# Kernel optimization log

Measured on AMD Instinct MI355X. Metric: run time of the kernel, lower is better.

## Reference

```python
import jax, jax.numpy as jnp
import numpy as np

LOCAL_REGION = 16
GRANULARITY = 2048
INIT_RATIO = 8
EXPAND_RATIO = 2
C = 128
N_LAYERS = 5


def setup_inputs() -> dict:
    key = jax.random.key(0)
    ks = jax.random.split(key, 20)
    g = lambda k, s: jax.random.normal(k, s, dtype=jnp.float32) * 0.05
    z = lambda n: jnp.zeros((n,), jnp.float32)
    return {
        "batch_x": jax.random.normal(ks[0], (1, 16384, 4), dtype=jnp.float32),
        # PT: attr embedding (in_channel=1 -> 128), positional MLP (3->128->128)
        "attr_w": g(ks[1], (1, C)), "attr_b": z(C),
        "pos_w1": g(ks[2], (3, C)), "pos_b1": z(C),
        "pos_w2": g(ks[3], (C, C)), "pos_b2": z(C),
        # 5 self-attention layers over the K-neighborhood
        "wq": g(ks[4], (N_LAYERS, C, C)),
        "wk": g(ks[5], (N_LAYERS, C, C)),
        "wv": g(ks[6], (N_LAYERS, C, C)),
        "wout": g(ks[7], (C, C)), "bout": z(C),
        # mu/sigma head: 128 -> 64 -> 16 -> 2
        "ms_w1": g(ks[8], (C, 64)), "ms_b1": z(64),
        "ms_w2": g(ks[9], (64, 16)), "ms_b2": z(16),
        "ms_w3": g(ks[10], (16, 2)), "ms_b3": z(2),
    }


def _window_schedule(N):
    base = min(N // INIT_RATIO, GRANULARITY)
    win = base
    sched = []
    cursor = base
    while cursor < N:
        win = min(win * EXPAND_RATIO, GRANULARITY)
        sched.append((cursor, min(win, N - cursor)))
        cursor += win
    return sched


def _forward(batch_x, attr_w, attr_b, pos_w1, pos_b1, pos_w2, pos_b2,
             wq, wk, wv, wout, bout, ms_w1, ms_b1, ms_w2, ms_b2, ms_w3, ms_b3):
    B, N, _ = batch_x.shape
    total_bits = jnp.float32(0.0)
    for cur, w in _window_schedule(N):
        context = batch_x[:, :cur, :]
        target = batch_x[:, cur:cur + w, :]
        tg, ta = target[..., :3], target[..., 3:]    # [B,M,3], [B,M,1]
        cg, ca = context[..., :3], context[..., 3:]  # [B,Nc,3], [B,Nc,1]
        # knn_points: brute-force squared distances, K smallest
        d2 = (jnp.sum(tg * tg, -1)[:, :, None] + jnp.sum(cg * cg, -1)[:, None, :]
              - 2.0 * jnp.einsum('bmd,bnd->bmn', tg, cg))  # [B,M,Nc]
        _, idx = jax.lax.top_k(-d2, LOCAL_REGION)            # [B,M,K]
        # knn_gather
        gg = jnp.take_along_axis(cg[:, None], idx[..., None], axis=2)  # [B,M,K,3]
        ga = jnp.take_along_axis(ca[:, None], idx[..., None], axis=2)  # [B,M,K,1]
        # n_scale_ball: center each neighborhood, scale into unit ball
        gg = gg - jnp.mean(gg, axis=2, keepdims=True)
        r = jnp.max(jnp.linalg.norm(gg, axis=-1, keepdims=True), axis=2, keepdims=True)
        gg = gg / jnp.maximum(r, 1e-8)
        # PT: pos-encoded grouped self-attention, max-pool over K
        pos = jax.nn.relu(gg @ pos_w1 + pos_b1) @ pos_w2 + pos_b2  # [B,M,K,C]
        f = ga @ attr_w + attr_b + pos
        for l in range(N_LAYERS):
            q, k, v = f @ wq[l], f @ wk[l], f @ wv[l]
            a = jax.nn.softmax(jnp.einsum('bmkc,bmjc->bmkj', q, k)
                               / jnp.sqrt(jnp.float32(C)), axis=-1)
            f = f + jnp.einsum('bmkj,bmjc->bmkc', a, v)
        feat = jnp.max(f @ wout + bout, axis=2)  # [B,M,C]
        # mu/sigma head
        h = jax.nn.relu(feat @ ms_w1 + ms_b1)
        h = jax.nn.relu(h @ ms_w2 + ms_b2)
        ms = h @ ms_w3 + ms_b3
        mu, sigma = ms[..., :1], jnp.exp(ms[..., 1:])
        # feature_probs_based_mu_sigma: bits under quantized Gaussian
        inv = 1.0 / (sigma * jnp.sqrt(jnp.float32(2.0)))
        probs = 0.5 * (jax.lax.erf((ta + 0.5 - mu) * inv)
                       - jax.lax.erf((ta - 0.5 - mu) * inv))
        total_bits = total_bits + jnp.sum(jnp.clip(-jnp.log2(probs + 1e-10), 0.0, 50.0))
    return total_bits


def reference(batch_x, attr_w, attr_b, pos_w1, pos_b1, pos_w2, pos_b2,
              wq, wk, wv, wout, bout, ms_w1, ms_b1, ms_w2, ms_b2, ms_w3, ms_b3):
    return _forward(batch_x, attr_w, attr_b, pos_w1, pos_b1, pos_w2, pos_b2,
                    wq, wk, wv, wout, bout, ms_w1, ms_b1, ms_w2, ms_b2, ms_w3, ms_b3)
```

## Files before the change

kernel.cpp:

```cpp
#include <hip/hip_runtime.h>
#include <math.h>

#define NPTS 16384
#define WWIN 2048
#define NWIN 7
#define KNB  16
#define CDIM 128
#define NTGT (NPTS - WWIN)
#define TPB  4
#define NBLK (NTGT / TPB)
#define NMAT 12

typedef _Float16 f16;
typedef __attribute__((ext_vector_type(8))) _Float16 f16x8;
typedef __attribute__((ext_vector_type(4))) _Float16 f16x4;
typedef __attribute__((ext_vector_type(2))) _Float16 f16x2;
typedef __attribute__((ext_vector_type(4))) float f32x4;

#define MFMA16(a, b, c) __builtin_amdgcn_mfma_f32_16x16x32_f16((a), (b), (c), 0, 0, 0)

__device__ __forceinline__ unsigned umax_(unsigned a, unsigned b) { return a > b ? a : b; }
__device__ __forceinline__ unsigned umin_(unsigned a, unsigned b) { return a < b ? a : b; }

__global__ void prep_kernel(const float* __restrict__ pos_w2,
                            const float* __restrict__ wq,
                            const float* __restrict__ wk,
                            const float* __restrict__ wv,
                            const float* __restrict__ wout,
                            f16* __restrict__ wt) {
  const int i = blockIdx.x * 256 + threadIdx.x;
  if (i >= NMAT * 16384) return;
  const int mat = i >> 14;
  const int e   = i & 16383;
  const int k   = e >> 7;
  const int n   = e & 127;
  if (mat < 7) {
    const float* src = (mat == 0) ? pos_w2 : (mat <= 5 ? wv + (mat - 1) * 16384 : wout);
    wt[mat * 16384 + n * 128 + k] = (f16)src[k * 128 + n];
  } else {
    const int l = mat - 7;
    const float* qr = wq + l * 16384 + k * 128;
    const float* kr = wk + l * 16384 + n * 128;
    float sacc = 0.f;
#pragma unroll 4
    for (int c = 0; c < 128; ++c) sacc += qr[c] * kr[c];
    wt[mat * 16384 + n * 128 + k] = (f16)sacc;
  }
}

__device__ __forceinline__ f16x8 ldA(const f16* __restrict__ buf, int row0,
                                     int l15, int lg, int kc) {
  const int row = row0 + l15;
  const int col = (kc * 32 + lg * 8) ^ ((row & 7) << 3);
  return *(const f16x8*)(buf + row * 128 + col);
}

__device__ __forceinline__ void stD(f16* __restrict__ buf, int row0, int col0,
                                    int l15, int lg, const f32x4 v) {
#pragma unroll
  for (int r = 0; r < 4; ++r) {
    const int row = row0 + lg * 4 + r;
    const int col = (col0 + l15) ^ ((row & 7) << 3);
    buf[row * 128 + col] = (f16)v[r];
  }
}

__device__ __forceinline__ void zacc(f32x4 (&acc)[4][2]) {
#pragma unroll
  for (int mt = 0; mt < 4; ++mt)
#pragma unroll
    for (int nt = 0; nt < 2; ++nt) acc[mt][nt] = (f32x4){0.f, 0.f, 0.f, 0.f};
}

__device__ __forceinline__ void gemm_tile(const f16* __restrict__ src,
                                          const f16* __restrict__ wmat,
                                          int l15, int lg, int n0,
                                          f32x4 (&acc)[4][2]) {
#pragma unroll
  for (int kc = 0; kc < 4; ++kc) {
    const f16x8 b0 = *(const f16x8*)(wmat + (n0 + l15) * 128 + kc * 32 + lg * 8);
    const f16x8 b1 = *(const f16x8*)(wmat + (n0 + 16 + l15) * 128 + kc * 32 + lg * 8);
#pragma unroll
    for (int mt = 0; mt < 4; ++mt) {
      const f16x8 a = ldA(src, mt * 16, l15, lg, kc);
      acc[mt][0] = MFMA16(a, b0, acc[mt][0]);
      acc[mt][1] = MFMA16(a, b1, acc[mt][1]);
    }
  }
}

__global__ __launch_bounds__(256, 2)
void nn_kernel(
    const float4* __restrict__ bx, const f16* __restrict__ wt,
    const float* __restrict__ attr_w, const float* __restrict__ attr_b,
    const float* __restrict__ pos_w1, const float* __restrict__ pos_b1,
    const float* __restrict__ pos_b2, const float* __restrict__ bout,
    const float* __restrict__ ms_w1, const float* __restrict__ ms_b1,
    const float* __restrict__ ms_w2, const float* __restrict__ ms_b2,
    const float* __restrict__ ms_w3, const float* __restrict__ ms_b3,
    float* __restrict__ partials) {
  __shared__ __align__(16) f16 fA[64 * 128];
  __shared__ __align__(16) f16 qA[64 * 128];
  __shared__ __align__(16) f16 vtB[128 * 64];
  __shared__ __align__(16) char aux[4096];

  const int t     = threadIdx.x;
  const int wv    = t >> 6;
  const int lane  = t & 63;
  const int l15   = lane & 15;
  const int lg    = lane >> 4;
  const int n0    = wv * 32;
  const int slot0 = (NBLK - 1 - blockIdx.x) * TPB;

  f16* pA = (f16*)aux;
  unsigned* nbr = (unsigned*)aux;
  float* ggs = (float*)(aux + 1024);

  {
    const int  slot = slot0 + wv;
    const int  cur  = WWIN * ((slot0 >> 11) + 1);
    const float4 tp = bx[WWIN + slot];

    unsigned u0 = 0xFFFFFFF0u, u1 = 0xFFFFFFF1u, u2 = 0xFFFFFFF2u, u3 = 0xFFFFFFF3u;

#define INS4(P) { const unsigned p_ = (P);                                     \
    const unsigned t0 = umax_(u0, p_); u0 = umin_(u0, p_);                     \
    const unsigned t1 = umax_(u1, t0); u1 = umin_(u1, t0);                     \
    const unsigned t2 = umax_(u2, t1); u2 = umin_(u2, t1);                     \
    u3 = umin_(u3, t2); }
#define PROC(CA, CB, JJ) {                                                     \
    const float dx0 = tp.x - (CA).x, dy0 = tp.y - (CA).y, dz0 = tp.z - (CA).z; \
    const float dx1 = tp.x - (CB).x, dy1 = tp.y - (CB).y, dz1 = tp.z - (CB).z; \
    const float d20 = dx0 * dx0 + dy0 * dy0 + dz0 * dz0;                       \
    const float d21 = dx1 * dx1 + dy1 * dy1 + dz1 * dz1;                       \
    const unsigned p0 = ((__float_as_uint(d20) << 1) & 0xFFFFC000u) | (unsigned)(JJ);      \
    const unsigned p1 = ((__float_as_uint(d21) << 1) & 0xFFFFC000u) | (unsigned)((JJ) + 64); \
    INS4(p0) INS4(p1) }

    float4 a0 = bx[lane],       b0 = bx[lane + 64];
    float4 a1 = bx[lane + 128], b1 = bx[lane + 192];
    float4 a2 = bx[lane + 256], b2 = bx[lane + 320];
    float4 a3 = bx[lane + 384], b3 = bx[lane + 448];
    for (int j = lane; j < cur; j += 512) {
      const float4 n0_ = bx[j + 512], n1_ = bx[j + 576];
      const float4 n2_ = bx[j + 640], n3_ = bx[j + 704];
      const float4 n4_ = bx[j + 768], n5_ = bx[j + 832];
      const float4 n6_ = bx[j + 896], n7_ = bx[j + 960];
      PROC(a0, b0, j)       a0 = n0_; b0 = n1_;
      PROC(a1, b1, j + 128) a1 = n2_; b1 = n3_;
      PROC(a2, b2, j + 256) a2 = n4_; b2 = n5_;
      PROC(a3, b3, j + 384) a3 = n6_; b3 = n7_;
    }
#undef PROC
#undef INS4

    for (int n = 0; n < 16; ++n) {
      unsigned m = u0;
      m = umin_(m, (unsigned)__shfl_xor((int)m, 1));
      m = umin_(m, (unsigned)__shfl_xor((int)m, 2));
      m = umin_(m, (unsigned)__shfl_xor((int)m, 4));
      m = umin_(m, (unsigned)__shfl_xor((int)m, 8));
      m = umin_(m, (unsigned)__shfl_xor((int)m, 16));
      m = umin_(m, (unsigned)__shfl_xor((int)m, 32));
      if (lane == n) nbr[wv * 16 + n] = m & 0x3FFFu;
      if (u0 == m) { u0 = u1; u1 = u2; u2 = u3; u3 = 0xFFFFFFFFu; }
    }
  }
  __syncthreads();

  if (t < 64) {
    const int nid  = (int)nbr[t];
    const float4 p = bx[nid];
    float sx = p.x, sy = p.y, sz = p.z;
#pragma unroll
    for (int m = 1; m < 16; m <<= 1) {
      sx += __shfl_xor(sx, m); sy += __shfl_xor(sy, m); sz += __shfl_xor(sz, m);
    }
    const float gx = p.x - sx * 0.0625f;
    const float gy = p.y - sy * 0.0625f;
    const float gz = p.z - sz * 0.0625f;
    float nr = sqrtf(gx * gx + gy * gy + gz * gz);
#pragma unroll
    for (int m = 1; m < 16; m <<= 1) nr = fmaxf(nr, __shfl_xor(nr, m));
    const float inv = 1.f / fmaxf(nr, 1e-8f);
    ggs[t * 4 + 0] = gx * inv; ggs[t * 4 + 1] = gy * inv;
    ggs[t * 4 + 2] = gz * inv; ggs[t * 4 + 3] = p.w;
  }
  __syncthreads();

  {
    const int row = t & 63;
    const int cb  = (t >> 6) * 32;
    const float gx = ggs[row * 4], gy = ggs[row * 4 + 1], gz = ggs[row * 4 + 2];
#pragma unroll
    for (int c = cb; c < cb + 32; c += 2) {
      const float h0 = pos_b1[c]     + gx * pos_w1[c]     + gy * pos_w1[128 + c]     + gz * pos_w1[256 + c];
      const float h1 = pos_b1[c + 1] + gx * pos_w1[c + 1] + gy * pos_w1[128 + c + 1] + gz * pos_w1[256 + c + 1];
      f16x2 pr; pr[0] = (f16)fmaxf(h0, 0.f); pr[1] = (f16)fmaxf(h1, 0.f);
      *(f16x2*)(qA + row * 128 + (c ^ ((row & 7) << 3))) = pr;
    }
  }
  __syncthreads();

  {
    f32x4 acc[4][2];
    zacc(acc);
    gemm_tile(qA, wt, l15, lg, n0, acc);
#pragma unroll
    for (int nt = 0; nt < 2; ++nt) {
      const int col = n0 + nt * 16 + l15;
      const float bias = pos_b2[col] + attr_b[col];
      const float aw   = attr_w[col];
#pragma unroll
      for (int mt = 0; mt < 4; ++mt) {
        f32x4 v = acc[mt][nt];
#pragma unroll
        for (int r = 0; r < 4; ++r)
          v[r] += bias + ggs[(mt * 16 + lg * 4 + r) * 4 + 3] * aw;
        stD(fA, mt * 16, n0 + nt * 16, l15, lg, v);
      }
    }
  }
  __syncthreads();

  f32x4 facc8[8];
#pragma unroll
  for (int nt = 0; nt < 8; ++nt) {
    const int col = nt * 16 + l15;
#pragma unroll
    for (int r = 0; r < 4; ++r) {
      const int row = wv * 16 + lg * 4 + r;
      facc8[nt][r] = (float)fA[row * 128 + (col ^ ((row & 7) << 3))];
    }
  }
  *(f16x8*)(pA + t * 8) = (f16x8){0, 0, 0, 0, 0, 0, 0, 0};

  for (int l = 0; l < 5; ++l) {
    {
      f32x4 acc[4][2];
      zacc(acc);
      gemm_tile(fA, wt + (7 + l) * 16384, l15, lg, n0, acc);
#pragma unroll
      for (int mt = 0; mt < 4; ++mt)
#pragma unroll
        for (int nt = 0; nt < 2; ++nt)
          stD(qA, mt * 16, n0 + nt * 16, l15, lg, acc[mt][nt]);
      zacc(acc);
      gemm_tile(fA, wt + (1 + l) * 16384, l15, lg, n0, acc);
#pragma unroll
      for (int mt = 0; mt < 4; ++mt)
#pragma unroll
        for (int nt = 0; nt < 2; ++nt) {
          const int ch = n0 + nt * 16 + l15;
          const int r0 = (mt * 16 + lg * 4) ^ ((ch & 7) << 3);
          f16x4 p;
#pragma unroll
          for (int r = 0; r < 4; ++r) p[r] = (f16)acc[mt][nt][r];
          *(f16x4*)(vtB + ch * 64 + r0) = p;
        }
    }
    __syncthreads();
    {
      f32x4 s = (f32x4){0.f, 0.f, 0.f, 0.f};
#pragma unroll
      for (int kc = 0; kc < 4; ++kc)
        s = MFMA16(ldA(qA, wv * 16, l15, lg, kc), ldA(fA, wv * 16, l15, lg, kc), s);
#pragma unroll
      for (int r = 0; r < 4; ++r) {
        float v = s[r] * 0.08838834764831844055f;
        float mx = v;
#pragma unroll
        for (int m = 1; m < 16; m <<= 1) mx = fmaxf(mx, __shfl_xor(mx, m));
        const float e = __expf(v - mx);
        float sm = e;
#pragma unroll
        for (int m = 1; m < 16; m <<= 1) sm += __shfl_xor(sm, m);
        pA[wv * 512 + (lg * 4 + r) * 32 + l15] = (f16)(e / sm);
      }
      const f16x8 a = *(const f16x8*)(pA + wv * 512 + l15 * 32 + lg * 8);
#pragma unroll
      for (int nt = 0; nt < 8; ++nt) {
        const int ch = nt * 16 + l15;
        const int r0 = (wv * 16 + 8 * (lg & 1)) ^ ((ch & 7) << 3);
        const f16x8 b = *(const f16x8*)(vtB + ch * 64 + r0);
        facc8[nt] = MFMA16(a, b, facc8[nt]);
        stD(fA, wv * 16, nt * 16, l15, lg, facc8[nt]);
      }
    }
    __syncthreads();
  }

  float* feats = (float*)aux;
  float* h1s   = feats + 512;
  float* h2s   = h1s + 256;
  float* btmp  = h2s + 64;
  {
    f32x4 acc[4][2];
    zacc(acc);
    gemm_tile(fA, wt + 6 * 16384, l15, lg, n0, acc);
#pragma unroll
    for (int nt = 0; nt < 2; ++nt) {
      const int col = n0 + nt * 16 + l15;
      const float bo = bout[col];
#pragma unroll
      for (int mt = 0; mt < 4; ++mt) {
        const f32x4 v = acc[mt][nt];
        float m = fmaxf(fmaxf(v[0], v[1]), fmaxf(v[2], v[3])) + bo;
        m = fmaxf(m, __shfl_xor(m, 16));
        m = fmaxf(m, __shfl_xor(m, 32));
        if (lg == 0) feats[mt * 128 + col] = m;
      }
    }
  }
  __syncthreads();
  {
    const int tt = t >> 6, h = t & 63;
    float a = ms_b1[h];
#pragma unroll 4
    for (int c = 0; c < 128; ++c) a += feats[tt * 128 + c] * ms_w1[c * 64 + h];
    h1s[tt * 64 + h] = fmaxf(a, 0.f);
  }
  __syncthreads();
  if (t < 64) {
    const int tt = t >> 4, h = t & 15;
    float a = ms_b2[h];
#pragma unroll 4
    for (int c = 0; c < 64; ++c) a += h1s[tt * 64 + c] * ms_w2[c * 16 + h];
    h2s[tt * 16 + h] = fmaxf(a, 0.f);
  }
  __syncthreads();
  if (t < TPB) {
    float mu = ms_b3[0], lgs = ms_b3[1];
#pragma unroll
    for (int c = 0; c < 16; ++c) {
      mu  += h2s[t * 16 + c] * ms_w3[2 * c];
      lgs += h2s[t * 16 + c] * ms_w3[2 * c + 1];
    }
    const float sigma = expf(lgs);
    const float inv   = 1.f / (sigma * 1.41421356237309504880f);
    const float ta    = ((const float*)bx)[(WWIN + slot0 + t) * 4 + 3];
    const float p = 0.5f * (erff((ta + 0.5f - mu) * inv) - erff((ta - 0.5f - mu) * inv));
    float bits = -log2f(p + 1e-10f);
    btmp[t] = fminf(fmaxf(bits, 0.f), 50.f);
  }
  __syncthreads();
  if (t == 0) partials[blockIdx.x] = btmp[0] + btmp[1] + btmp[2] + btmp[3];
}

__global__ void reduce_kernel(const float* __restrict__ partials, float* __restrict__ out) {
  float s = 0.f;
  for (int i = threadIdx.x; i < NBLK; i += 256) s += partials[i];
#pragma unroll
  for (int m = 1; m < 64; m <<= 1) s += __shfl_xor(s, m);
  __shared__ float wsum[4];
  if ((threadIdx.x & 63) == 0) wsum[threadIdx.x >> 6] = s;
  __syncthreads();
  if (threadIdx.x == 0) out[0] = wsum[0] + wsum[1] + wsum[2] + wsum[3];
}

extern "C" void kernel_launch(void* const* d_in, const int* in_sizes, int n_in,
                              void* d_out, int out_size, void* d_ws, size_t ws_size,
                              hipStream_t stream) {
  const float4* bx     = (const float4*)d_in[0];
  const float* attr_w  = (const float*)d_in[1];
  const float* attr_b  = (const float*)d_in[2];
  const float* pos_w1  = (const float*)d_in[3];
  const float* pos_b1  = (const float*)d_in[4];
  const float* pos_w2  = (const float*)d_in[5];
  const float* pos_b2  = (const float*)d_in[6];
  const float* wq      = (const float*)d_in[7];
  const float* wk      = (const float*)d_in[8];
  const float* wv      = (const float*)d_in[9];
  const float* wout    = (const float*)d_in[10];
  const float* bout    = (const float*)d_in[11];
  const float* ms_w1   = (const float*)d_in[12];
  const float* ms_b1   = (const float*)d_in[13];
  const float* ms_w2   = (const float*)d_in[14];
  const float* ms_b2   = (const float*)d_in[15];
  const float* ms_w3   = (const float*)d_in[16];
  const float* ms_b3   = (const float*)d_in[17];

  f16*   wt       = (f16*)((char*)d_ws);
  float* partials = (float*)((char*)d_ws + (1u << 19));

  prep_kernel<<<(NMAT * 16384 + 255) / 256, 256, 0, stream>>>(pos_w2, wq, wk, wv, wout, wt);
  nn_kernel<<<NBLK, 256, 0, stream>>>(bx, wt, attr_w, attr_b,
                                      pos_w1, pos_b1, pos_b2, bout,
                                      ms_w1, ms_b1, ms_w2, ms_b2, ms_w3, ms_b3,
                                      partials);
  reduce_kernel<<<1, 256, 0, stream>>>(partials, (float*)d_out);
}
```

Before: 365.0 us.

## Keep V in registers and use 16x16x16 MFMA for attention-weighted sum

Drops the transposed V shared-memory buffer. Each wave now keeps its own V tile columns in registers as f16 fragments and applies the per-target 16x16 softmax matrices through the 16x16x16 MFMA, so the residual accumulators follow the GEMM column split instead of the row split. This removes the vtB LDS writes and reads and frees LDS, which may help occupancy. The cost is an extra barrier per layer, more live registers, and a lower-throughput MFMA shape.

```diff
diff --git a/kernel.cpp b/kernel.cpp
--- a/kernel.cpp
+++ b/kernel.cpp
@@ -17,7 +17,8 @@
 typedef __attribute__((ext_vector_type(2))) _Float16 f16x2;
 typedef __attribute__((ext_vector_type(4))) float f32x4;
 
-#define MFMA16(a, b, c) __builtin_amdgcn_mfma_f32_16x16x32_f16((a), (b), (c), 0, 0, 0)
+#define MFMA16(a, b, c)  __builtin_amdgcn_mfma_f32_16x16x32_f16((a), (b), (c), 0, 0, 0)
+#define MFMA16H(a, b, c) __builtin_amdgcn_mfma_f32_16x16x16f16((a), (b), (c), 0, 0, 0)
 
 __device__ __forceinline__ unsigned umax_(unsigned a, unsigned b) { return a > b ? a : b; }
 __device__ __forceinline__ unsigned umin_(unsigned a, unsigned b) { return a < b ? a : b; }
@@ -101,7 +102,6 @@
     float* __restrict__ partials) {
   __shared__ __align__(16) f16 fA[64 * 128];
   __shared__ __align__(16) f16 qA[64 * 128];
-  __shared__ __align__(16) f16 vtB[128 * 64];
   __shared__ __align__(16) char aux[4096];
 
   const int t     = threadIdx.x;
@@ -112,7 +112,7 @@
   const int n0    = wv * 32;
   const int slot0 = (NBLK - 1 - blockIdx.x) * TPB;
 
-  f16* pA = (f16*)aux;
+  f16* pAh = (f16*)aux;
   unsigned* nbr = (unsigned*)aux;
   float* ggs = (float*)(aux + 1024);
 
@@ -202,10 +202,10 @@
   }
   __syncthreads();
 
-  {
-    f32x4 acc[4][2];
-    zacc(acc);
-    gemm_tile(qA, wt, l15, lg, n0, acc);
+  f32x4 facc[4][2];
+  {
+    zacc(facc);
+    gemm_tile(qA, wt, l15, lg, n0, facc);
 #pragma unroll
     for (int nt = 0; nt < 2; ++nt) {
       const int col = n0 + nt * 16 + l15;
@@ -213,29 +213,17 @@
       const float aw   = attr_w[col];
 #pragma unroll
       for (int mt = 0; mt < 4; ++mt) {
-        f32x4 v = acc[mt][nt];
 #pragma unroll
         for (int r = 0; r < 4; ++r)
-          v[r] += bias + ggs[(mt * 16 + lg * 4 + r) * 4 + 3] * aw;
-        stD(fA, mt * 16, n0 + nt * 16, l15, lg, v);
+          facc[mt][nt][r] += bias + ggs[(mt * 16 + lg * 4 + r) * 4 + 3] * aw;
+        stD(fA, mt * 16, n0 + nt * 16, l15, lg, facc[mt][nt]);
       }
     }
   }
   __syncthreads();
 
-  f32x4 facc8[8];
-#pragma unroll
-  for (int nt = 0; nt < 8; ++nt) {
-    const int col = nt * 16 + l15;
-#pragma unroll
-    for (int r = 0; r < 4; ++r) {
-      const int row = wv * 16 + lg * 4 + r;
-      facc8[nt][r] = (float)fA[row * 128 + (col ^ ((row & 7) << 3))];
-    }
-  }
-  *(f16x8*)(pA + t * 8) = (f16x8){0, 0, 0, 0, 0, 0, 0, 0};
-
   for (int l = 0; l < 5; ++l) {
+    f16x4 vfrag[4][2];
     {
       f32x4 acc[4][2];
       zacc(acc);
@@ -250,14 +238,10 @@
 #pragma unroll
       for (int mt = 0; mt < 4; ++mt)
 #pragma unroll
-        for (int nt = 0; nt < 2; ++nt) {
-          const int ch = n0 + nt * 16 + l15;
-          const int r0 = (mt * 16 + lg * 4) ^ ((ch & 7) << 3);
-          f16x4 p;
-#pragma unroll
-          for (int r = 0; r < 4; ++r) p[r] = (f16)acc[mt][nt][r];
-          *(f16x4*)(vtB + ch * 64 + r0) = p;
-        }
+        for (int nt = 0; nt < 2; ++nt)
+#pragma unroll
+        for (int r = 0; r < 4; ++r)
+          vfrag[mt][nt][r] = (f16)acc[mt][nt][r];
     }
     __syncthreads();
     {
@@ -275,16 +259,19 @@
         float sm = e;
 #pragma unroll
         for (int m = 1; m < 16; m <<= 1) sm += __shfl_xor(sm, m);
-        pA[wv * 512 + (lg * 4 + r) * 32 + l15] = (f16)(e / sm);
+        pAh[wv * 256 + (lg * 4 + r) * 16 + l15] = (f16)(e / sm);
       }
-      const f16x8 a = *(const f16x8*)(pA + wv * 512 + l15 * 32 + lg * 8);
-#pragma unroll
-      for (int nt = 0; nt < 8; ++nt) {
-        const int ch = nt * 16 + l15;
-        const int r0 = (wv * 16 + 8 * (lg & 1)) ^ ((ch & 7) << 3);
-        const f16x8 b = *(const f16x8*)(vtB + ch * 64 + r0);
-        facc8[nt] = MFMA16(a, b, facc8[nt]);
-        stD(fA, wv * 16, nt * 16, l15, lg, facc8[nt]);
+    }
+    __syncthreads();
+    {
+#pragma unroll
+      for (int tt = 0; tt < 4; ++tt) {
+        const f16x4 aP = *(const f16x4*)(pAh + tt * 256 + l15 * 16 + lg * 4);
+#pragma unroll
+        for (int nt = 0; nt < 2; ++nt) {
+          facc[tt][nt] = MFMA16H(aP, vfrag[tt][nt], facc[tt][nt]);
+          stD(fA, tt * 16, n0 + nt * 16, l15, lg, facc[tt][nt]);
+        }
       }
     }
     __syncthreads();
```

Result: no change. 361.8 us (median of 2 runs) (-0.9%).
